# Optimization experiments

Measured on AMD Instinct MI355X. Metric: run time of the kernel, lower is better.

## Reference

```python
import jax, jax.numpy as jnp
import numpy as np

# tcnn HashGrid config from ntc_conf
L = 16            # n_levels
T = 1 << 15       # 2**log2_hashmap_size entries per level
F = 4             # n_features_per_level
BASE = 16.0       # base_resolution
N_PTS = 1_000_000
PRIMES = jnp.array([1, 2654435761, 805459861], dtype=jnp.uint32)  # tcnn spatial hash primes
OFFS = np.array([[(c >> 2) & 1, (c >> 1) & 1, c & 1] for c in range(8)], dtype=np.uint32)  # 8 cube corners


def hash_encode(x, table):
    """Multi-resolution hash grid encoding. x: [N,3] in [0,1], table: [L,T,F] -> [N, L*F]."""
    N = x.shape[0]
    scales = BASE * (2.0 ** jnp.arange(L, dtype=jnp.float32))        # [L]
    pos = x[:, None, :] * scales[None, :, None]                      # [N,L,3]
    p0 = jnp.floor(pos)
    frac = pos - p0                                                  # trilinear weights source
    p0u = p0.astype(jnp.uint32)
    flat_table = table.reshape(L * T, F)
    level_off = (jnp.arange(L, dtype=jnp.uint32) * jnp.uint32(T))[None, :]  # [1,L]
    acc = jnp.zeros((N, L, F), dtype=table.dtype)
    for c in range(8):  # fixed 8 corners -> keeps peak memory at [N,L,F] per corner
        off = jnp.asarray(OFFS[c])                                   # [3] uint32
        corner = p0u + off                                           # [N,L,3]
        h = corner * PRIMES                                          # uint32 wraparound mul
        idx = (h[..., 0] ^ h[..., 1] ^ h[..., 2]) & jnp.uint32(T - 1)  # [N,L]
        feats = flat_table[(idx + level_off).astype(jnp.int32)]      # gather [N,L,F]
        w = jnp.prod(jnp.where(off.astype(bool), frac, 1.0 - frac), axis=-1)  # [N,L]
        acc = acc + w[..., None] * feats
    return acc.reshape(N, L * F)


def setup_inputs() -> dict:
    key = jax.random.key(0)
    k1, k2, k3, k4, k5 = jax.random.split(key, 5)
    xyz = jax.random.normal(k1, (N_PTS, 3), dtype=jnp.float32)
    xyz_bound_min = -jnp.ones((3,), dtype=jnp.float32)
    xyz_bound_max = jnp.ones((3,), dtype=jnp.float32)
    hash_table = jax.random.normal(k2, (L, T, F), dtype=jnp.float32) * 1e-2  # tcnn-style small init
    w0 = jax.random.normal(k3, (64, 64), dtype=jnp.float32) * (1.0 / 8.0)
    w1 = jax.random.normal(k4, (64, 64), dtype=jnp.float32) * (1.0 / 8.0)
    w2 = jax.random.normal(k5, (64, 8), dtype=jnp.float32) * (1.0 / 8.0)
    return {"xyz": xyz, "xyz_bound_min": xyz_bound_min, "xyz_bound_max": xyz_bound_max,
            "hash_table": hash_table, "w0": w0, "w1": w1, "w2": w2}


def reference(xyz, xyz_bound_min, xyz_bound_max, hash_table, w0, w1, w2):
    contracted = (xyz - xyz_bound_min) / (xyz_bound_max - xyz_bound_min)   # [N,3]
    mask = jnp.all((contracted >= 0.0) & (contracted <= 1.0), axis=1)      # [N]
    # Evaluate on all points (clamped) and mask the writes -- equivalent to the
    # original compaction (contracted[mask]) + scatter-back, jit-friendly shapes.
    xin = jnp.clip(contracted, 0.0, 1.0)
    enc = hash_encode(xin, hash_table)                                     # [N,64]
    h = jax.nn.relu(enc @ w0)
    h = jax.nn.relu(h @ w1)
    resi = h @ w2                                                          # [N,8]
    d_xyz = jnp.where(mask[:, None], resi[:, :3], 0.0)
    ident_rot = jnp.array([1.0, 0.0, 0.0, 0.0], dtype=resi.dtype)
    d_rot = jnp.where(mask[:, None], resi[:, 3:7], ident_rot)
    return mask, d_xyz, d_rot
```

## Files before the change

kernel.cpp:

```cpp
#include <hip/hip_runtime.h>
#include <hip/hip_bf16.h>


#define LVL 16
#define TSZ 32768
#define PR1 2654435761u
#define PR2 805459861u
#define SUBS 32
#define STRIDE (SUBS * 1024)

typedef __attribute__((ext_vector_type(8))) short bf16x8;
typedef __attribute__((ext_vector_type(4))) float f32x4;
typedef __attribute__((ext_vector_type(2))) float f32x2;
typedef __attribute__((ext_vector_type(4))) unsigned short u16x4;
typedef __attribute__((ext_vector_type(2))) unsigned int u32x2;
typedef long long i64;

__device__ __forceinline__ unsigned short f2bf(float f) {
    return __builtin_bit_cast(unsigned short, __float2bfloat16(f));
}

__device__ __forceinline__ int hswz(int kt, int pt) {
    return (kt * 4096 + pt * 16) ^ (((pt >> 2) & 3) << 5) ^ ((kt & 1) << 4);
}

__device__ __forceinline__ unsigned f32x4_to_fp8x4(float f0, float f1, float f2, float f3) {
#if __has_builtin(__builtin_amdgcn_cvt_pk_fp8_f32)
    int u = 0;
    u = __builtin_amdgcn_cvt_pk_fp8_f32(f0, f1, u, false);
    u = __builtin_amdgcn_cvt_pk_fp8_f32(f2, f3, u, true);
    return (unsigned)u;
#else
    float ff[4] = { f0, f1, f2, f3 };
    unsigned u = 0;
    for (int k = 0; k < 4; ++k) {
        const float v = ff[k];
        const unsigned s = v < 0.f ? 1u : 0u;
        float av = fabsf(v);
        unsigned b;
        if (av < 6.103515625e-05f) {
            b = 0u;
        } else if (av < 0.015625f) {
            b = (unsigned)rintf(av * 512.f);
        } else {
            int e; float m = frexpf(av, &e);
            unsigned E = (unsigned)(e - 1 + 7);
            unsigned q = (unsigned)rintf(m * 16.f);
            if (q == 16u) { q = 8u; ++E; }
            b = (E << 3) | (q - 8u);
        }
        u |= ((s << 7) | b) << (8 * k);
    }
    return u;
#endif
}

__device__ __forceinline__ unsigned char f32_to_fp8(float v) {
    return (unsigned char)(f32x4_to_fp8x4(v, v, v, v) & 0xffu);
}

__device__ __forceinline__ void fp8x4_to_2f32x2(unsigned r, f32x2& lo, f32x2& hi) {
#if __has_builtin(__builtin_amdgcn_cvt_pk_f32_fp8)
    lo = __builtin_amdgcn_cvt_pk_f32_fp8((int)r, false);
    hi = __builtin_amdgcn_cvt_pk_f32_fp8((int)r, true);
#else
    float f[4];
#pragma unroll
    for (int k = 0; k < 4; ++k) {
        const unsigned b = (r >> (8 * k)) & 0xffu;
        const unsigned s = b >> 7, em = b & 0x7fu, e = em >> 3, m = em & 7u;
        float v;
        if (e) v = __builtin_bit_cast(float, ((e + 120u) << 23) | (m << 20));
        else   v = (float)m * 0.001953125f;
        f[k] = s ? -v : v;
    }
    lo = (f32x2){ f[0], f[1] };
    hi = (f32x2){ f[2], f[3] };
#endif
}

__global__ __launch_bounds__(256) void k_tbl8(
    const float* __restrict__ t, unsigned* __restrict__ o, int n4,
    const float* __restrict__ w0, const float* __restrict__ w1,
    const float* __restrict__ w2, char* __restrict__ wbase)
{
    const int g = blockIdx.x * 256 + threadIdx.x;
    if (g < n4) {
        const float4 a = reinterpret_cast<const float4*>(t)[g];
        o[g] = f32x4_to_fp8x4(a.x * 256.f, a.y * 256.f, a.z * 256.f, a.w * 256.f);
    }
    if (blockIdx.x == gridDim.x - 1) {
        const int tt = threadIdx.x;
        unsigned char*  wf8 = (unsigned char*)wbase;
        unsigned short* wf1 = (unsigned short*)(wbase + 4096);
        unsigned short* wf2 = (unsigned short*)(wbase + 4096 + 8192);
#pragma unroll
        for (int q = 0; q < 16; ++q) {
            const int s = q * 256 + tt;
            const int e = s & 7, f = s >> 3;
            const int ln = f & 63, ntkk = f >> 6;
            const int k = (ntkk & 1) * 32 + (ln >> 4) * 8 + e;
            const int n = (ntkk >> 1) * 16 + (ln & 15);
            wf8[s] = f32_to_fp8(w0[k * 64 + n]);
        }
#pragma unroll
        for (int q = 0; q < 16; ++q) {
            const int s = q * 256 + tt;
            const int e = s & 7, f = s >> 3;
            const int ln = f & 63, ntkk = f >> 6;
            const int k = (ntkk & 1) * 32 + (ln >> 4) * 8 + e;
            const int n = (ntkk >> 1) * 16 + (ln & 15);
            wf1[s] = f2bf(w1[k * 64 + n]);
        }
#pragma unroll
        for (int q = 0; q < 4; ++q) {
            const int s = q * 256 + tt;
            const int e = s & 7, f = s >> 3;
            const int ln = f & 63, kk = f >> 6;
            const int k = kk * 32 + (ln >> 4) * 8 + e;
            const int n = ln & 15;
            wf2[s] = (n < 8) ? f2bf(w2[k * 8 + n]) : (unsigned short)0;
        }
    }
}

__global__ __launch_bounds__(1024) void k_enc(
    const float* __restrict__ xyz, const float* __restrict__ bmin, const float* __restrict__ bmax,
    const unsigned* __restrict__ tbl8, float* __restrict__ out,
    unsigned* __restrict__ enc, int N, int Npad)
{
    __shared__ unsigned tabL[TSZ];

    const int t   = threadIdx.x;
    const int l   = blockIdx.x & 15;
    const int sub = blockIdx.x >> 4;

    {
        const uint4* __restrict__ src = reinterpret_cast<const uint4*>(tbl8 + (size_t)l * TSZ);
        uint4* dst = reinterpret_cast<uint4*>(tabL);
#pragma unroll
        for (int j = 0; j < 8; ++j) dst[j * 1024 + t] = src[j * 1024 + t];
    }
    __syncthreads();

    const float bx0 = bmin[0], by0 = bmin[1], bz0 = bmin[2];
    const float iex = 1.f / (bmax[0] - bx0);
    const float iey = 1.f / (bmax[1] - by0);
    const float iez = 1.f / (bmax[2] - bz0);
    const float scale = 16.f * (float)(1u << l);
    unsigned* __restrict__ encL = enc + (size_t)l * Npad;
    const bool isL0 = (l == 0);

    const unsigned PR1_4 = PR1 << 2;
    const unsigned PR2_4 = PR2 << 2;
    const unsigned M2 = (TSZ - 1u) << 2;

    int p = sub * 1024 + t;
    if (p < Npad) {
        int pc = p < N ? p : N - 1;
        float cxr = xyz[3 * pc + 0], cyr = xyz[3 * pc + 1], czr = xyz[3 * pc + 2];

        for (; p < Npad; ) {
            const int pn  = p + STRIDE;
            const int pnc = pn < N ? pn : N - 1;
            const float nxr = xyz[3 * pnc + 0];
            const float nyr = xyz[3 * pnc + 1];
            const float nzr = xyz[3 * pnc + 2];

            const float ccx = (cxr - bx0) * iex;
            const float ccy = (cyr - by0) * iey;
            const float ccz = (czr - bz0) * iez;
            if (isL0 && p < N) {
                const bool inside = (ccx >= 0.f) && (ccx <= 1.f) && (ccy >= 0.f) &&
                                    (ccy <= 1.f) && (ccz >= 0.f) && (ccz <= 1.f);
                out[p] = inside ? 1.f : 0.f;
            }
            const float x = fminf(fmaxf(ccx, 0.f), 1.f);
            const float y = fminf(fmaxf(ccy, 0.f), 1.f);
            const float z = fminf(fmaxf(ccz, 0.f), 1.f);

            const float px = x * scale, py = y * scale, pz = z * scale;
            const float fx = floorf(px), fy = floorf(py), fz = floorf(pz);
            const float rx = px - fx, ry = py - fy, rz = pz - fz;
            const unsigned ux = (unsigned)fx, uy = (unsigned)fy, uz = (unsigned)fz;

            const unsigned ux4 = ux << 2;
            const unsigned hy4 = uy * PR1_4, hz4 = uz * PR2_4;
            const unsigned hxy2[4] = {
                (ux4        ^ hy4)           & M2,
                (ux4        ^ (hy4 + PR1_4)) & M2,
                ((ux4 + 4u) ^ hy4)           & M2,
                ((ux4 + 4u) ^ (hy4 + PR1_4)) & M2 };
            const unsigned hz2[2] = { hz4 & M2, (hz4 + PR2_4) & M2 };

            const float wx0 = 1.f - rx, wy0 = 1.f - ry, wz0 = 1.f - rz;
            const f32x2 wyp = { wy0, ry };
            const f32x2 wxyA = (f32x2){ wx0, wx0 } * wyp;
            const f32x2 wxyB = (f32x2){ rx,  rx  } * wyp;
            const f32x2 wz2 = { wz0, rz };
            const f32x2 w8[4] = {
                (f32x2){ wxyA[0], wxyA[0] } * wz2,
                (f32x2){ wxyA[1], wxyA[1] } * wz2,
                (f32x2){ wxyB[0], wxyB[0] } * wz2,
                (f32x2){ wxyB[1], wxyB[1] } * wz2 };

            unsigned r[8];
#pragma unroll
            for (int c = 0; c < 8; ++c)
                r[c] = *reinterpret_cast<const unsigned*>(
                    reinterpret_cast<const char*>(tabL) + (hxy2[c >> 1] ^ hz2[c & 1]));

            f32x2 a01 = { 0.f, 0.f }, a23 = { 0.f, 0.f };
#pragma unroll
            for (int c = 0; c < 8; ++c) {
                f32x2 lo, hi;
                fp8x4_to_2f32x2(r[c], lo, hi);
                const float w = w8[c >> 1][c & 1];
                const f32x2 w2 = { w, w };
                a01 += w2 * lo;
                a23 += w2 * hi;
            }

            const unsigned v = f32x4_to_fp8x4(a01[0], a01[1], a23[0], a23[1]);
            __builtin_nontemporal_store(v, encL + p);

            p = pn; cxr = nxr; cyr = nyr; czr = nzr;
        }
    }
}

__global__ __launch_bounds__(256) void k_mlp(
    const char* __restrict__ wbase, const unsigned* __restrict__ enc,
    float* __restrict__ out, int N, int Npad)
{
    __shared__ __align__(16) char hTb[32768];

    const unsigned char*  wf8 = (const unsigned char*)wbase;
    const unsigned short* wf1 = (const unsigned short*)(wbase + 4096);
    const unsigned short* wf2 = (const unsigned short*)(wbase + 4096 + 8192);

    const int t = threadIdx.x, wv = t >> 6, ln = t & 63;
    const int col = ln & 15, g = ln >> 4;
    const int ptb = blockIdx.x * 256;
    const int i = ptb + t;

    u32x2 a0[2][4];
#pragma unroll
    for (int kk = 0; kk < 2; ++kk)
#pragma unroll
        for (int mt = 0; mt < 4; ++mt) {
            const size_t pt = (size_t)ptb + wv * 64 + mt * 16 + col;
            const int j = kk * 4 + g;
            u32x2 a;
            a[0] = __builtin_nontemporal_load(enc + (size_t)(2 * j)     * Npad + pt);
            a[1] = __builtin_nontemporal_load(enc + (size_t)(2 * j + 1) * Npad + pt);
            a0[kk][mt] = a;
        }
    u32x2 b0[4][2];
#pragma unroll
    for (int nt = 0; nt < 4; ++nt)
#pragma unroll
        for (int kk = 0; kk < 2; ++kk)
            b0[nt][kk] = *reinterpret_cast<const u32x2*>(wf8 + ((nt * 2 + kk) * 64 + ln) * 8);

    f32x4 acc[4][4];
#pragma unroll
    for (int mt = 0; mt < 4; ++mt)
#pragma unroll
        for (int nt = 0; nt < 4; ++nt) acc[mt][nt] = (f32x4){0.f, 0.f, 0.f, 0.f};

#pragma unroll
    for (int kk = 0; kk < 2; ++kk)
#pragma unroll
        for (int nt = 0; nt < 4; ++nt)
#pragma unroll
            for (int mt = 0; mt < 4; ++mt)
                acc[mt][nt] = __builtin_amdgcn_mfma_f32_16x16x32_fp8_fp8(
                    __builtin_bit_cast(i64, a0[kk][mt]),
                    __builtin_bit_cast(i64, b0[nt][kk]), acc[mt][nt], 0, 0, 0);

#pragma unroll
    for (int mt = 0; mt < 4; ++mt)
#pragma unroll
        for (int nt = 0; nt < 4; ++nt) {
            const int kt = nt * 2 + (col >> 3), j = col & 7;
#pragma unroll
            for (int r = 0; r < 4; ++r) {
                const int pt = wv * 64 + mt * 16 + g * 4 + r;
                *reinterpret_cast<unsigned short*>(hTb + hswz(kt, pt) + 2 * j) =
                    f2bf(fmaxf(acc[mt][nt][r], 0.f) * 0.00390625f);
            }
        }

    bf16x8 b1[4][2];
#pragma unroll
    for (int nt = 0; nt < 4; ++nt)
#pragma unroll
        for (int kk = 0; kk < 2; ++kk)
            b1[nt][kk] = *reinterpret_cast<const bf16x8*>(wf1 + ((nt * 2 + kk) * 64 + ln) * 8);

#pragma unroll
    for (int mt = 0; mt < 4; ++mt)
#pragma unroll
        for (int nt = 0; nt < 4; ++nt) acc[mt][nt] = (f32x4){0.f, 0.f, 0.f, 0.f};

#pragma unroll
    for (int kk = 0; kk < 2; ++kk) {
        bf16x8 a[4];
#pragma unroll
        for (int mt = 0; mt < 4; ++mt)
            a[mt] = *reinterpret_cast<const bf16x8*>(
                hTb + hswz(kk * 4 + g, wv * 64 + mt * 16 + col));
#pragma unroll
        for (int nt = 0; nt < 4; ++nt)
#pragma unroll
            for (int mt = 0; mt < 4; ++mt)
                acc[mt][nt] = __builtin_amdgcn_mfma_f32_16x16x32_bf16(a[mt], b1[nt][kk], acc[mt][nt], 0, 0, 0);
    }

#pragma unroll
    for (int mt = 0; mt < 4; ++mt)
#pragma unroll
        for (int nt = 0; nt < 4; ++nt) {
            const int kt = nt * 2 + (col >> 3), j = col & 7;
#pragma unroll
            for (int r = 0; r < 4; ++r) {
                const int pt = wv * 64 + mt * 16 + g * 4 + r;
                *reinterpret_cast<unsigned short*>(hTb + hswz(kt, pt) + 2 * j) =
                    f2bf(fmaxf(acc[mt][nt][r], 0.f));
            }
        }

    f32x4 acc2[4];
#pragma unroll
    for (int mt = 0; mt < 4; ++mt) acc2[mt] = (f32x4){0.f, 0.f, 0.f, 0.f};

#pragma unroll
    for (int kk = 0; kk < 2; ++kk) {
        const bf16x8 b2 = *reinterpret_cast<const bf16x8*>(wf2 + (kk * 64 + ln) * 8);
        bf16x8 a[4];
#pragma unroll
        for (int mt = 0; mt < 4; ++mt)
            a[mt] = *reinterpret_cast<const bf16x8*>(
                hTb + hswz(kk * 4 + g, wv * 64 + mt * 16 + col));
#pragma unroll
        for (int mt = 0; mt < 4; ++mt)
            acc2[mt] = __builtin_amdgcn_mfma_f32_16x16x32_bf16(a[mt], b2, acc2[mt], 0, 0, 0);
    }

    __syncthreads();
    float* resS = reinterpret_cast<float*>(hTb);
    if (col < 8) {
#pragma unroll
        for (int mt = 0; mt < 4; ++mt)
#pragma unroll
            for (int r = 0; r < 4; ++r)
                resS[(wv * 64 + mt * 16 + g * 4 + r) * 8 + col] = acc2[mt][r];
    }
    __syncthreads();

    if (i < N) {
        const bool inside = (out[i] != 0.f);
        const f32x4 lo = *reinterpret_cast<f32x4*>(&resS[t * 8 + 0]);
        const f32x4 hi = *reinterpret_cast<f32x4*>(&resS[t * 8 + 4]);

        float* __restrict__ dxyz = out + N;
        dxyz[3 * i + 0] = inside ? lo.x : 0.f;
        dxyz[3 * i + 1] = inside ? lo.y : 0.f;
        dxyz[3 * i + 2] = inside ? lo.z : 0.f;

        float4* __restrict__ drot = reinterpret_cast<float4*>(out + 4 * (size_t)N);
        drot[i] = inside ? make_float4(lo.w, hi.x, hi.y, hi.z)
                         : make_float4(1.f, 0.f, 0.f, 0.f);
    }
}

__global__ __launch_bounds__(256) void ntc_fused(
    const float* __restrict__ xyz, const float* __restrict__ bmin, const float* __restrict__ bmax,
    const float* __restrict__ table, const float* __restrict__ w0, const float* __restrict__ w1,
    const float* __restrict__ w2, float* __restrict__ out, int N)
{
    __shared__ unsigned short encT[8 * 256 * 8];
    __shared__ unsigned short w0t[64 * 64];
    __shared__ unsigned short w1t[64 * 64];
    __shared__ unsigned short w2t[16 * 64];

    const int t = threadIdx.x, wv = t >> 6, ln = t & 63;
    const int col = ln & 15, g = ln >> 4;

#pragma unroll
    for (int it = 0; it < 16; ++it) {
        const int idx = it * 256 + t;
        const int k = idx >> 6, n = idx & 63;
        w0t[n * 64 + k] = f2bf(w0[idx]);
        w1t[n * 64 + k] = f2bf(w1[idx]);
    }
#pragma unroll
    for (int q = 0; q < 4; ++q) {
        const int idx = t * 4 + q;
        const int n = idx >> 6, k = idx & 63;
        w2t[idx] = (n < 8) ? f2bf(w2[k * 8 + n]) : (unsigned short)0;
    }

    const int i = blockIdx.x * 256 + t;
    const int ic = (i < N) ? i : (N - 1);
    const float bx0 = bmin[0], by0 = bmin[1], bz0 = bmin[2];
    const float ex = bmax[0] - bx0, ey = bmax[1] - by0, ez = bmax[2] - bz0;
    const float cx = (xyz[3 * ic + 0] - bx0) / ex;
    const float cy = (xyz[3 * ic + 1] - by0) / ey;
    const float cz = (xyz[3 * ic + 2] - bz0) / ez;
    const bool inside = (cx >= 0.f) && (cx <= 1.f) && (cy >= 0.f) && (cy <= 1.f) &&
                        (cz >= 0.f) && (cz <= 1.f);
    const float x = fminf(fmaxf(cx, 0.f), 1.f);
    const float y = fminf(fmaxf(cy, 0.f), 1.f);
    const float z = fminf(fmaxf(cz, 0.f), 1.f);
    const float4* __restrict__ tab = reinterpret_cast<const float4*>(table);

    for (int l = 0; l < LVL; ++l) {
        const float scale = 16.f * (float)(1u << l);
        const float px = x * scale, py = y * scale, pz = z * scale;
        const float fx = floorf(px), fy = floorf(py), fz = floorf(pz);
        const float rx = px - fx, ry = py - fy, rz = pz - fz;
        const unsigned ux = (unsigned)fx, uy = (unsigned)fy, uz = (unsigned)fz;
        const unsigned hx[2] = { ux, ux + 1u };
        const unsigned hy[2] = { uy * PR1, (uy + 1u) * PR1 };
        const unsigned hz[2] = { uz * PR2, (uz + 1u) * PR2 };
        const float wx[2] = { 1.f - rx, rx };
        const float wy[2] = { 1.f - ry, ry };
        const float wz[2] = { 1.f - rz, rz };
        float a0 = 0.f, a1 = 0.f, a2 = 0.f, a3 = 0.f;
#pragma unroll
        for (int c = 0; c < 8; ++c) {
            const int ox = (c >> 2) & 1, oy = (c >> 1) & 1, oz = c & 1;
            const unsigned idx = (hx[ox] ^ hy[oy] ^ hz[oz]) & (TSZ - 1u);
            const float4 f4 = tab[l * TSZ + idx];
            const float w = wx[ox] * wy[oy] * wz[oz];
            a0 = fmaf(w, f4.x, a0); a1 = fmaf(w, f4.y, a1);
            a2 = fmaf(w, f4.z, a2); a3 = fmaf(w, f4.w, a3);
        }
        u16x4 v = { f2bf(a0), f2bf(a1), f2bf(a2), f2bf(a3) };
        *reinterpret_cast<u16x4*>(&encT[(l >> 1) * 2048 + t * 8 + (l & 1) * 4]) = v;
    }
    __syncthreads();

    f32x4 acc[4][4];
#pragma unroll
    for (int mt = 0; mt < 4; ++mt)
#pragma unroll
        for (int nt = 0; nt < 4; ++nt) acc[mt][nt] = (f32x4){0.f, 0.f, 0.f, 0.f};
#pragma unroll
    for (int kk = 0; kk < 2; ++kk) {
        bf16x8 a[4];
#pragma unroll
        for (int mt = 0; mt < 4; ++mt)
            a[mt] = *reinterpret_cast<bf16x8*>(&encT[(kk * 4 + g) * 2048 + (wv * 64 + mt * 16 + col) * 8]);
#pragma unroll
        for (int nt = 0; nt < 4; ++nt) {
            bf16x8 b = *reinterpret_cast<bf16x8*>(&w0t[(nt * 16 + col) * 64 + kk * 32 + g * 8]);
#pragma unroll
            for (int mt = 0; mt < 4; ++mt)
                acc[mt][nt] = __builtin_amdgcn_mfma_f32_16x16x32_bf16(a[mt], b, acc[mt][nt], 0, 0, 0);
        }
    }
    __syncthreads();
#pragma unroll
    for (int mt = 0; mt < 4; ++mt)
#pragma unroll
        for (int nt = 0; nt < 4; ++nt) {
            const int kt = nt * 2 + (col >> 3), j = col & 7;
#pragma unroll
            for (int r = 0; r < 4; ++r)
                encT[kt * 2048 + (wv * 64 + mt * 16 + g * 4 + r) * 8 + j] = f2bf(fmaxf(acc[mt][nt][r], 0.f));
        }
    __syncthreads();
#pragma unroll
    for (int mt = 0; mt < 4; ++mt)
#pragma unroll
        for (int nt = 0; nt < 4; ++nt) acc[mt][nt] = (f32x4){0.f, 0.f, 0.f, 0.f};
#pragma unroll
    for (int kk = 0; kk < 2; ++kk) {
        bf16x8 a[4];
#pragma unroll
        for (int mt = 0; mt < 4; ++mt)
            a[mt] = *reinterpret_cast<bf16x8*>(&encT[(kk * 4 + g) * 2048 + (wv * 64 + mt * 16 + col) * 8]);
#pragma unroll
        for (int nt = 0; nt < 4; ++nt) {
            bf16x8 b = *reinterpret_cast<bf16x8*>(&w1t[(nt * 16 + col) * 64 + kk * 32 + g * 8]);
#pragma unroll
            for (int mt = 0; mt < 4; ++mt)
                acc[mt][nt] = __builtin_amdgcn_mfma_f32_16x16x32_bf16(a[mt], b, acc[mt][nt], 0, 0, 0);
        }
    }
    __syncthreads();
#pragma unroll
    for (int mt = 0; mt < 4; ++mt)
#pragma unroll
        for (int nt = 0; nt < 4; ++nt) {
            const int kt = nt * 2 + (col >> 3), j = col & 7;
#pragma unroll
            for (int r = 0; r < 4; ++r)
                encT[kt * 2048 + (wv * 64 + mt * 16 + g * 4 + r) * 8 + j] = f2bf(fmaxf(acc[mt][nt][r], 0.f));
        }
    __syncthreads();
    f32x4 acc2[4];
#pragma unroll
    for (int mt = 0; mt < 4; ++mt) acc2[mt] = (f32x4){0.f, 0.f, 0.f, 0.f};
#pragma unroll
    for (int kk = 0; kk < 2; ++kk) {
        bf16x8 a[4];
#pragma unroll
        for (int mt = 0; mt < 4; ++mt)
            a[mt] = *reinterpret_cast<bf16x8*>(&encT[(kk * 4 + g) * 2048 + (wv * 64 + mt * 16 + col) * 8]);
        bf16x8 b = *reinterpret_cast<bf16x8*>(&w2t[col * 64 + kk * 32 + g * 8]);
#pragma unroll
        for (int mt = 0; mt < 4; ++mt)
            acc2[mt] = __builtin_amdgcn_mfma_f32_16x16x32_bf16(a[mt], b, acc2[mt], 0, 0, 0);
    }
    __syncthreads();
    float* res = reinterpret_cast<float*>(encT);
    if (col < 8) {
#pragma unroll
        for (int mt = 0; mt < 4; ++mt)
#pragma unroll
            for (int r = 0; r < 4; ++r)
                res[(wv * 64 + mt * 16 + g * 4 + r) * 8 + col] = acc2[mt][r];
    }
    __syncthreads();
    if (i < N) {
        const f32x4 lo = *reinterpret_cast<f32x4*>(&res[t * 8 + 0]);
        const f32x4 hi = *reinterpret_cast<f32x4*>(&res[t * 8 + 4]);
        out[i] = inside ? 1.f : 0.f;
        float* __restrict__ dxyz = out + N;
        dxyz[3 * i + 0] = inside ? lo.x : 0.f;
        dxyz[3 * i + 1] = inside ? lo.y : 0.f;
        dxyz[3 * i + 2] = inside ? lo.z : 0.f;
        float4* __restrict__ drot = reinterpret_cast<float4*>(out + 4 * (size_t)N);
        drot[i] = inside ? make_float4(lo.w, hi.x, hi.y, hi.z)
                         : make_float4(1.f, 0.f, 0.f, 0.f);
    }
}

extern "C" void kernel_launch(void* const* d_in, const int* in_sizes, int n_in,
                              void* d_out, int out_size, void* d_ws, size_t ws_size,
                              hipStream_t stream) {
    const float* xyz   = (const float*)d_in[0];
    const float* bmin  = (const float*)d_in[1];
    const float* bmax  = (const float*)d_in[2];
    const float* table = (const float*)d_in[3];
    const float* w0    = (const float*)d_in[4];
    const float* w1    = (const float*)d_in[5];
    const float* w2    = (const float*)d_in[6];
    float* out = (float*)d_out;

    const int N = in_sizes[0] / 3;
    const int nb = (N + 255) / 256;
    const int Npad = ((N + 4095) / 4096) * 4096;
    const int tblElems = in_sizes[3];

    size_t offW = ((size_t)tblElems + 63) & ~(size_t)63;
    size_t offEnc = (offW + 14336 + 255) & ~(size_t)255;
    size_t need = offEnc + (size_t)Npad * 64;

    if (ws_size >= need) {
        unsigned* tbl8 = (unsigned*)d_ws;
        char* wbase    = (char*)d_ws + offW;
        unsigned* enc  = (unsigned*)((char*)d_ws + offEnc);
        const int n4 = tblElems / 4;
        k_tbl8<<<(n4 + 255) / 256, 256, 0, stream>>>(table, tbl8, n4, w0, w1, w2, wbase);
        k_enc<<<16 * SUBS, 1024, 0, stream>>>(xyz, bmin, bmax, tbl8, out, enc, N, Npad);
        k_mlp<<<nb, 256, 0, stream>>>(wbase, enc, out, N, Npad);
    } else {
        ntc_fused<<<nb, 256, 0, stream>>>(xyz, bmin, bmax, table, w0, w1, w2, out, N);
    }
}
```

Before: 188.2 us.

## Fuse table fp8 conversion into encoder kernel and drop LDS swizzle in MLP

Removes the separate table-conversion kernel: each encoder block now reads its level's fp32 table slice and converts to fp8 directly into shared memory, with the last block also packing the MLP weights. The per-level subgrid count is halved so fewer blocks redundantly convert the same table, and Npad shrinks to a multiple of 256. The MLP kernel replaces the swizzled shared buffer with a plain layout plus a separate result buffer, dropping a barrier but risking LDS bank conflicts. The weight packing now runs inside an encoder block while k_mlp reads it, which relies on kernel ordering in the stream.

```diff
diff --git a/kernel.cpp b/kernel.cpp
--- a/kernel.cpp
+++ b/kernel.cpp
@@ -6,7 +6,7 @@
 #define TSZ 32768
 #define PR1 2654435761u
 #define PR2 805459861u
-#define SUBS 32
+#define SUBS 16
 #define STRIDE (SUBS * 1024)
 
 typedef __attribute__((ext_vector_type(8))) short bf16x8;
@@ -18,10 +18,6 @@
 
 __device__ __forceinline__ unsigned short f2bf(float f) {
     return __builtin_bit_cast(unsigned short, __float2bfloat16(f));
-}
-
-__device__ __forceinline__ int hswz(int kt, int pt) {
-    return (kt * 4096 + pt * 16) ^ (((pt >> 2) & 3) << 5) ^ ((kt & 1) << 4);
 }
 
 __device__ __forceinline__ unsigned f32x4_to_fp8x4(float f0, float f1, float f2, float f3) {
@@ -79,67 +75,53 @@
 #endif
 }
 
-__global__ __launch_bounds__(256) void k_tbl8(
-    const float* __restrict__ t, unsigned* __restrict__ o, int n4,
+__global__ __launch_bounds__(1024) void k_enc(
+    const float* __restrict__ xyz, const float* __restrict__ bmin, const float* __restrict__ bmax,
+    const float* __restrict__ table, float* __restrict__ out,
+    unsigned* __restrict__ enc, int N, int Npad,
     const float* __restrict__ w0, const float* __restrict__ w1,
     const float* __restrict__ w2, char* __restrict__ wbase)
 {
-    const int g = blockIdx.x * 256 + threadIdx.x;
-    if (g < n4) {
-        const float4 a = reinterpret_cast<const float4*>(t)[g];
-        o[g] = f32x4_to_fp8x4(a.x * 256.f, a.y * 256.f, a.z * 256.f, a.w * 256.f);
-    }
-    if (blockIdx.x == gridDim.x - 1) {
-        const int tt = threadIdx.x;
+    __shared__ unsigned tabL[TSZ];
+
+    const int t   = threadIdx.x;
+    const int l   = blockIdx.x & 15;
+    const int sub = blockIdx.x >> 4;
+
+    {
+        const float4* __restrict__ src =
+            reinterpret_cast<const float4*>(table + (size_t)l * TSZ * 4);
+#pragma unroll 4
+        for (int j = 0; j < 32; ++j) {
+            const int idx = j * 1024 + t;
+            const float4 a = src[idx];
+            tabL[idx] = f32x4_to_fp8x4(a.x * 256.f, a.y * 256.f, a.z * 256.f, a.w * 256.f);
+        }
+    }
+
+    if (blockIdx.x == 16 * SUBS - 1 && t < 256) {
         unsigned char*  wf8 = (unsigned char*)wbase;
         unsigned short* wf1 = (unsigned short*)(wbase + 4096);
         unsigned short* wf2 = (unsigned short*)(wbase + 4096 + 8192);
 #pragma unroll
         for (int q = 0; q < 16; ++q) {
-            const int s = q * 256 + tt;
+            const int s = q * 256 + t;
             const int e = s & 7, f = s >> 3;
             const int ln = f & 63, ntkk = f >> 6;
             const int k = (ntkk & 1) * 32 + (ln >> 4) * 8 + e;
             const int n = (ntkk >> 1) * 16 + (ln & 15);
             wf8[s] = f32_to_fp8(w0[k * 64 + n]);
-        }
-#pragma unroll
-        for (int q = 0; q < 16; ++q) {
-            const int s = q * 256 + tt;
-            const int e = s & 7, f = s >> 3;
-            const int ln = f & 63, ntkk = f >> 6;
-            const int k = (ntkk & 1) * 32 + (ln >> 4) * 8 + e;
-            const int n = (ntkk >> 1) * 16 + (ln & 15);
             wf1[s] = f2bf(w1[k * 64 + n]);
         }
 #pragma unroll
         for (int q = 0; q < 4; ++q) {
-            const int s = q * 256 + tt;
+            const int s = q * 256 + t;
             const int e = s & 7, f = s >> 3;
             const int ln = f & 63, kk = f >> 6;
             const int k = kk * 32 + (ln >> 4) * 8 + e;
             const int n = ln & 15;
             wf2[s] = (n < 8) ? f2bf(w2[k * 8 + n]) : (unsigned short)0;
         }
-    }
-}
-
-__global__ __launch_bounds__(1024) void k_enc(
-    const float* __restrict__ xyz, const float* __restrict__ bmin, const float* __restrict__ bmax,
-    const unsigned* __restrict__ tbl8, float* __restrict__ out,
-    unsigned* __restrict__ enc, int N, int Npad)
-{
-    __shared__ unsigned tabL[TSZ];
-
-    const int t   = threadIdx.x;
-    const int l   = blockIdx.x & 15;
-    const int sub = blockIdx.x >> 4;
-
-    {
-        const uint4* __restrict__ src = reinterpret_cast<const uint4*>(tbl8 + (size_t)l * TSZ);
-        uint4* dst = reinterpret_cast<uint4*>(tabL);
-#pragma unroll
-        for (int j = 0; j < 8; ++j) dst[j * 1024 + t] = src[j * 1024 + t];
     }
     __syncthreads();
 
@@ -162,7 +144,7 @@
 
         for (; p < Npad; ) {
             const int pn  = p + STRIDE;
-            const int pnc = pn < N ? pn : N - 1;
+            const int pnc = (pn < N) ? pn : (N - 1);
             const float nxr = xyz[3 * pnc + 0];
             const float nyr = xyz[3 * pnc + 1];
             const float nzr = xyz[3 * pnc + 2];
@@ -233,7 +215,8 @@
     const char* __restrict__ wbase, const unsigned* __restrict__ enc,
     float* __restrict__ out, int N, int Npad)
 {
-    __shared__ __align__(16) char hTb[32768];
+    __shared__ unsigned short hT[8 * 256 * 8];
+    __shared__ float resS[256 * 8];
 
     const unsigned char*  wf8 = (const unsigned char*)wbase;
     const unsigned short* wf1 = (const unsigned short*)(wbase + 4096);
@@ -285,11 +268,9 @@
         for (int nt = 0; nt < 4; ++nt) {
             const int kt = nt * 2 + (col >> 3), j = col & 7;
 #pragma unroll
-            for (int r = 0; r < 4; ++r) {
-                const int pt = wv * 64 + mt * 16 + g * 4 + r;
-                *reinterpret_cast<unsigned short*>(hTb + hswz(kt, pt) + 2 * j) =
+            for (int r = 0; r < 4; ++r)
+                hT[kt * 2048 + (wv * 64 + mt * 16 + g * 4 + r) * 8 + j] =
                     f2bf(fmaxf(acc[mt][nt][r], 0.f) * 0.00390625f);
-            }
         }
 
     bf16x8 b1[4][2];
@@ -309,8 +290,8 @@
         bf16x8 a[4];
 #pragma unroll
         for (int mt = 0; mt < 4; ++mt)
-            a[mt] = *reinterpret_cast<const bf16x8*>(
-                hTb + hswz(kk * 4 + g, wv * 64 + mt * 16 + col));
+            a[mt] = *reinterpret_cast<bf16x8*>(
+                &hT[(kk * 4 + g) * 2048 + (wv * 64 + mt * 16 + col) * 8]);
 #pragma unroll
         for (int nt = 0; nt < 4; ++nt)
 #pragma unroll
@@ -324,11 +305,9 @@
         for (int nt = 0; nt < 4; ++nt) {
             const int kt = nt * 2 + (col >> 3), j = col & 7;
 #pragma unroll
-            for (int r = 0; r < 4; ++r) {
-                const int pt = wv * 64 + mt * 16 + g * 4 + r;
-                *reinterpret_cast<unsigned short*>(hTb + hswz(kt, pt) + 2 * j) =
+            for (int r = 0; r < 4; ++r)
+                hT[kt * 2048 + (wv * 64 + mt * 16 + g * 4 + r) * 8 + j] =
                     f2bf(fmaxf(acc[mt][nt][r], 0.f));
-            }
         }
 
     f32x4 acc2[4];
@@ -341,15 +320,13 @@
         bf16x8 a[4];
 #pragma unroll
         for (int mt = 0; mt < 4; ++mt)
-            a[mt] = *reinterpret_cast<const bf16x8*>(
-                hTb + hswz(kk * 4 + g, wv * 64 + mt * 16 + col));
+            a[mt] = *reinterpret_cast<bf16x8*>(
+                &hT[(kk * 4 + g) * 2048 + (wv * 64 + mt * 16 + col) * 8]);
 #pragma unroll
         for (int mt = 0; mt < 4; ++mt)
             acc2[mt] = __builtin_amdgcn_mfma_f32_16x16x32_bf16(a[mt], b2, acc2[mt], 0, 0, 0);
     }
 
-    __syncthreads();
-    float* resS = reinterpret_cast<float*>(hTb);
     if (col < 8) {
 #pragma unroll
         for (int mt = 0; mt < 4; ++mt)
@@ -554,20 +531,16 @@
 
     const int N = in_sizes[0] / 3;
     const int nb = (N + 255) / 256;
-    const int Npad = ((N + 4095) / 4096) * 4096;
-    const int tblElems = in_sizes[3];
-
-    size_t offW = ((size_t)tblElems + 63) & ~(size_t)63;
-    size_t offEnc = (offW + 14336 + 255) & ~(size_t)255;
+    const int Npad = nb * 256;
+
+    size_t offEnc = 14336;
     size_t need = offEnc + (size_t)Npad * 64;
 
     if (ws_size >= need) {
-        unsigned* tbl8 = (unsigned*)d_ws;
-        char* wbase    = (char*)d_ws + offW;
-        unsigned* enc  = (unsigned*)((char*)d_ws + offEnc);
-        const int n4 = tblElems / 4;
-        k_tbl8<<<(n4 + 255) / 256, 256, 0, stream>>>(table, tbl8, n4, w0, w1, w2, wbase);
-        k_enc<<<16 * SUBS, 1024, 0, stream>>>(xyz, bmin, bmax, tbl8, out, enc, N, Npad);
+        char* wbase   = (char*)d_ws;
+        unsigned* enc = (unsigned*)((char*)d_ws + offEnc);
+        k_enc<<<16 * SUBS, 1024, 0, stream>>>(xyz, bmin, bmax, table, out, enc, N, Npad,
+                                              w0, w1, w2, wbase);
         k_mlp<<<nb, 256, 0, stream>>>(wbase, enc, out, N, Npad);
     } else {
         ntc_fused<<<nb, 256, 0, stream>>>(xyz, bmin, bmax, table, w0, w1, w2, out, N);
```

After: 173.4 us. -7.9%, faster.
